# Kernel tuning notes

Measured on AMD Instinct MI355X. Metric: run time of the kernel, lower is better.

The kernel has to match this reference:

```python
import jax, jax.numpy as jnp
import numpy as np

REG1 = 0.5
REG2 = 0.5
ALPHA = 0.5

def setup_inputs() -> dict:
    key = jax.random.key(0)
    k1, k2, k3, k4, k5 = jax.random.split(key, 5)
    N, D, K = 32768, 256, 2048
    return {
        "encoder_out": jax.random.normal(k1, (N, D), dtype=jnp.float32),
        "prototypes": jax.random.normal(k2, (K, D), dtype=jnp.float32),
        "recon_loss": jax.random.uniform(k3, (), dtype=jnp.float32),
        "kl_loss": jax.random.uniform(k4, (), dtype=jnp.float32),
        "mmd_loss": jax.random.uniform(k5, (), dtype=jnp.float32),
    }


def _cdist_min_loss(z, prototypes):
    # torch.cdist(z, protos) -> [N, K]; f_dist = cdist(protos, z) = its transpose.
    # prototypes accessed via .data in torch -> detached.
    p = jax.lax.stop_gradient(prototypes)
    z2 = jnp.sum(z * z, axis=1, keepdims=True)          # [N, 1]
    p2 = jnp.sum(p * p, axis=1)                          # [K]
    sq = z2 + p2[None, :] - 2.0 * (z @ p.T)              # [N, K]
    dist = jnp.sqrt(jnp.maximum(sq, 0.0))
    p_min = jnp.min(dist, axis=1).mean()   # p_dist.min(1).values.mean()
    f_min = jnp.min(dist, axis=0).mean()   # f_dist [K,N].min(1) == dist.min(0)
    return REG1 * p_min + REG2 * f_min


def reference(encoder_out, prototypes, recon_loss, kl_loss, mmd_loss):
    cvae_loss = recon_loss + ALPHA * kl_loss + mmd_loss
    prot_decoding_loss = _cdist_min_loss(encoder_out, prototypes)
    # no projection head (use_projector=False)
    x = encoder_out / jnp.maximum(
        jnp.linalg.norm(encoder_out, axis=1, keepdims=True), 1e-12)
    x_mapped = x @ prototypes.T  # [N, K]
    return (encoder_out, x, x_mapped, cvae_loss, prot_decoding_loss)
```

## Files before the change

### kernel.cpp

```cpp
#include <hip/hip_runtime.h>
#include <hip/hip_bf16.h>

typedef __bf16 bf16x8 __attribute__((ext_vector_type(8)));
typedef __bf16 bf16x4 __attribute__((ext_vector_type(4)));
typedef float  f32x4  __attribute__((ext_vector_type(4)));

#define N_ROWS 32768
#define D_DIM  256
#define K_PROT 2048

#define WS_Z2    0
#define WS_INVN  32768
#define WS_P2    65536
#define WS_RMIN  67584
#define WS_CMIN  100352
#define WS_ZB    102400
#define WS_PB    (102400 + 4194304)

#define OUT_X0   0UL
#define OUT_X1   8388608UL
#define OUT_XMAP 16777216UL
#define OUT_CVAE 83886080UL
#define OUT_PROT 83886081UL

__device__ __forceinline__ void gload16(const __bf16* gsrc, const __bf16* ldst) {
    auto g = (const __attribute__((address_space(1))) unsigned int*)(unsigned long long)gsrc;
    auto l = (__attribute__((address_space(3))) unsigned int*)(unsigned long long)ldst;
    __builtin_amdgcn_global_load_lds(g, l, 16, 0, 0);
}

__global__ __launch_bounds__(256) void k12_rows(
    const float* __restrict__ Z, const float* __restrict__ P,
    float* __restrict__ out0, float* __restrict__ out1,
    float* __restrict__ z2, float* __restrict__ invn, unsigned int* __restrict__ rmin,
    __bf16* __restrict__ Zb,
    float* __restrict__ p2, unsigned int* __restrict__ cmin, __bf16* __restrict__ Pb)
{
    int b    = blockIdx.x;
    int lane = threadIdx.x & 63;
    if (b < (N_ROWS/4)) {
        int row  = (b << 2) + (threadIdx.x >> 6);
        size_t base = (size_t)row * D_DIM;
        float4 v = ((const float4*)(Z + base))[lane];
        float ss = v.x*v.x + v.y*v.y + v.z*v.z + v.w*v.w;
        #pragma unroll
        for (int d = 32; d >= 1; d >>= 1) ss += __shfl_xor(ss, d);
        float inv = 1.0f / fmaxf(sqrtf(ss), 1e-12f);
        ((float4*)(out0 + base))[lane] = v;
        float4 xv; xv.x = v.x*inv; xv.y = v.y*inv; xv.z = v.z*inv; xv.w = v.w*inv;
        ((float4*)(out1 + base))[lane] = xv;
        bf16x4 bv; bv[0]=(__bf16)v.x; bv[1]=(__bf16)v.y; bv[2]=(__bf16)v.z; bv[3]=(__bf16)v.w;
        ((bf16x4*)(Zb + base))[lane] = bv;
        if (lane == 0) { z2[row] = ss; invn[row] = inv; rmin[row] = 0x7f800000u; }
    } else {
        int row  = ((b - (N_ROWS/4)) << 2) + (threadIdx.x >> 6);
        size_t base = (size_t)row * D_DIM;
        float4 v = ((const float4*)(P + base))[lane];
        float ss = v.x*v.x + v.y*v.y + v.z*v.z + v.w*v.w;
        #pragma unroll
        for (int d = 32; d >= 1; d >>= 1) ss += __shfl_xor(ss, d);
        bf16x4 bv; bv[0]=(__bf16)v.x; bv[1]=(__bf16)v.y; bv[2]=(__bf16)v.z; bv[3]=(__bf16)v.w;
        ((bf16x4*)(Pb + base))[lane] = bv;
        if (lane == 0) { p2[row] = ss; cmin[row] = 0x7f800000u; }
    }
}

#define BM 128
#define BN 128
#define BK 64

__global__ __launch_bounds__(256, 2) void k3_gemm(
    const __bf16* __restrict__ Zb, const __bf16* __restrict__ Pb,
    const float* __restrict__ z2, const float* __restrict__ p2,
    const float* __restrict__ invn,
    float* __restrict__ xmap,
    unsigned int* __restrict__ rmin, unsigned int* __restrict__ cmin)
{
    __shared__ __bf16 As[BM * BK];
    __shared__ __bf16 Bs[BN * BK];

    const int tid  = threadIdx.x;
    const int wg   = (blockIdx.x & 7) * 512 + (blockIdx.x >> 3);
    const int bn   = wg & 15;
    const int bm   = wg >> 4;
    const int lane = tid & 63;
    const int wave = tid >> 6;
    const int wm   = wave >> 1;
    const int wn   = wave & 1;
    const int l15  = lane & 15;
    const int quad = lane >> 4;

    const int m0 = bm * BM;
    const int n0 = bn * BN;

    f32x4 acc[4][4];
    #pragma unroll
    for (int i = 0; i < 4; i++)
        #pragma unroll
        for (int j = 0; j < 4; j++)
            #pragma unroll
            for (int r = 0; r < 4; r++) acc[i][j][r] = 0.0f;

    const int ch_row[4] = {
        ((0*4 + wave)*64 + lane) >> 3, ((1*4 + wave)*64 + lane) >> 3,
        ((2*4 + wave)*64 + lane) >> 3, ((3*4 + wave)*64 + lane) >> 3 };
    const int ch_c = lane & 7;

    for (int kt = 0; kt < D_DIM; kt += BK) {
        #pragma unroll
        for (int it = 0; it < 4; it++) {
            const __bf16* aS = Zb + (size_t)(m0 + ch_row[it]) * D_DIM + kt + ch_c * 8;
            const __bf16* bS = Pb + (size_t)(n0 + ch_row[it]) * D_DIM + kt + ch_c * 8;
            gload16(aS, As + (it*4 + wave) * 512);
            gload16(bS, Bs + (it*4 + wave) * 512);
        }
        __syncthreads();

        #pragma unroll
        for (int s = 0; s < 2; s++) {
            bf16x8 af[4], bfr[4];
            #pragma unroll
            for (int i = 0; i < 4; i++)
                af[i] = *(const bf16x8*)(As + (wm*64 + i*16 + l15) * BK + s*32 + quad*8);
            #pragma unroll
            for (int j = 0; j < 4; j++)
                bfr[j] = *(const bf16x8*)(Bs + (wn*64 + j*16 + l15) * BK + s*32 + quad*8);
            #pragma unroll
            for (int i = 0; i < 4; i++)
                #pragma unroll
                for (int j = 0; j < 4; j++)
                    acc[i][j] = __builtin_amdgcn_mfma_f32_16x16x32_bf16(af[i], bfr[j], acc[i][j], 0, 0, 0);
        }
        __syncthreads();
    }

    float invr[16], zzr[16];
    #pragma unroll
    for (int i = 0; i < 4; i++)
        #pragma unroll
        for (int r = 0; r < 4; r++) {
            int gm = m0 + wm*64 + i*16 + quad*4 + r;
            invr[i*4+r] = invn[gm];
            zzr[i*4+r]  = z2[gm];
        }
    float pp[4];
    #pragma unroll
    for (int j = 0; j < 4; j++) pp[j] = p2[n0 + wn*64 + j*16 + l15];

    float cminv[4] = {3.0e38f, 3.0e38f, 3.0e38f, 3.0e38f};

    #pragma unroll
    for (int i = 0; i < 4; i++) {
        #pragma unroll
        for (int r = 0; r < 4; r++) {
            int gm = m0 + wm*64 + i*16 + quad*4 + r;
            float zi = zzr[i*4+r], iv = invr[i*4+r];
            size_t orow = (size_t)gm * K_PROT + n0 + wn*64 + l15;
            float rv = 3.0e38f;
            #pragma unroll
            for (int j = 0; j < 4; j++) {
                float g = acc[i][j][r];
                xmap[orow + j*16] = g * iv;
                float d2 = fmaxf(zi + pp[j] - 2.0f*g, 0.0f);
                rv = fminf(rv, d2);
                cminv[j] = fminf(cminv[j], d2);
            }
            #pragma unroll
            for (int s = 1; s < 16; s <<= 1) rv = fminf(rv, __shfl_xor(rv, s));
            if (l15 == 0) atomicMin(&rmin[gm], __float_as_uint(rv));
        }
    }
    #pragma unroll
    for (int j = 0; j < 4; j++) {
        float cv = cminv[j];
        cv = fminf(cv, __shfl_xor(cv, 16));
        cv = fminf(cv, __shfl_xor(cv, 32));
        if (quad == 0) atomicMin(&cmin[n0 + wn*64 + j*16 + l15], __float_as_uint(cv));
    }
}

__global__ __launch_bounds__(1024) void k4_final(
    const float* __restrict__ rminf, const float* __restrict__ cminf,
    const float* __restrict__ recon, const float* __restrict__ kl,
    const float* __restrict__ mmd, float* __restrict__ out)
{
    __shared__ float sr[16], sc[16];
    int tid = threadIdx.x;
    float a = 0.0f, b = 0.0f;
    for (int i = tid; i < N_ROWS; i += 1024) a += sqrtf(fmaxf(rminf[i], 0.0f));
    for (int i = tid; i < K_PROT; i += 1024) b += sqrtf(fmaxf(cminf[i], 0.0f));
    #pragma unroll
    for (int d = 32; d >= 1; d >>= 1) { a += __shfl_xor(a, d); b += __shfl_xor(b, d); }
    int w = tid >> 6, lane = tid & 63;
    if (lane == 0) { sr[w] = a; sc[w] = b; }
    __syncthreads();
    if (tid == 0) {
        float SA = 0.0f, SB = 0.0f;
        #pragma unroll
        for (int i = 0; i < 16; i++) { SA += sr[i]; SB += sc[i]; }
        out[OUT_CVAE] = recon[0] + 0.5f*kl[0] + mmd[0];
        out[OUT_PROT] = 0.5f*(SA / (float)N_ROWS) + 0.5f*(SB / (float)K_PROT);
    }
}

extern "C" void kernel_launch(void* const* d_in, const int* in_sizes, int n_in,
                              void* d_out, int out_size, void* d_ws, size_t ws_size,
                              hipStream_t stream)
{
    const float* Z     = (const float*)d_in[0];
    const float* P     = (const float*)d_in[1];
    const float* recon = (const float*)d_in[2];
    const float* kl    = (const float*)d_in[3];
    const float* mmd   = (const float*)d_in[4];
    float* out = (float*)d_out;
    float* ws  = (float*)d_ws;

    float* z2   = ws + WS_Z2;
    float* invn = ws + WS_INVN;
    float* p2   = ws + WS_P2;
    unsigned int* rmin = (unsigned int*)(ws + WS_RMIN);
    unsigned int* cmin = (unsigned int*)(ws + WS_CMIN);
    __bf16* Zb = (__bf16*)(ws + WS_ZB);
    __bf16* Pb = (__bf16*)(ws + WS_PB);

    hipLaunchKernelGGL(k12_rows, dim3(N_ROWS/4 + K_PROT/4), dim3(256), 0, stream,
                       Z, P, out + OUT_X0, out + OUT_X1, z2, invn, rmin, Zb, p2, cmin, Pb);
    hipLaunchKernelGGL(k3_gemm, dim3((N_ROWS/BM)*(K_PROT/BN)), dim3(256), 0, stream,
                       Zb, Pb, z2, p2, invn, out + OUT_XMAP, rmin, cmin);
    hipLaunchKernelGGL(k4_final, dim3(1), dim3(1024), 0, stream,
                       (const float*)rmin, (const float*)cmin, recon, kl, mmd, out);
}
```

Baseline: 437.3 us.

## Replace global atomicMin with per-tile partial minima and parallel reduction kernel

The GEMM epilogue no longer issues global atomicMin per row and column. Each block combines its wave partials in shared memory and writes per-tile row and column minima to workspace buffers. A new 80-block reduce kernel finishes the minima, takes sqrt, sums, and atomically adds into two accumulators, replacing the single-block final kernel. Launch bounds are raised to 3 blocks per CU, and one extra kernel launch is added along with about 4MB of partial-buffer traffic.

After: 432.7 us. No clear change (-1.1%).

```diff
diff --git a/kernel.cpp b/kernel.cpp
--- a/kernel.cpp
+++ b/kernel.cpp
@@ -12,10 +12,11 @@
 #define WS_Z2    0
 #define WS_INVN  32768
 #define WS_P2    65536
-#define WS_RMIN  67584
-#define WS_CMIN  100352
-#define WS_ZB    102400
-#define WS_PB    (102400 + 4194304)
+#define WS_ACC   67584
+#define WS_RP    67600
+#define WS_CP    (67600 + 524288)
+#define WS_ZB    (67600 + 1048576)
+#define WS_PB    (67600 + 1048576 + 4194304)
 
 #define OUT_X0   0UL
 #define OUT_X1   8388608UL
@@ -32,12 +33,14 @@
 __global__ __launch_bounds__(256) void k12_rows(
     const float* __restrict__ Z, const float* __restrict__ P,
     float* __restrict__ out0, float* __restrict__ out1,
-    float* __restrict__ z2, float* __restrict__ invn, unsigned int* __restrict__ rmin,
+    float* __restrict__ z2, float* __restrict__ invn,
     __bf16* __restrict__ Zb,
-    float* __restrict__ p2, unsigned int* __restrict__ cmin, __bf16* __restrict__ Pb)
+    float* __restrict__ p2, __bf16* __restrict__ Pb,
+    float* __restrict__ accw)
 {
     int b    = blockIdx.x;
     int lane = threadIdx.x & 63;
+    if (b == 0 && threadIdx.x < 2) accw[threadIdx.x] = 0.0f;
     if (b < (N_ROWS/4)) {
         int row  = (b << 2) + (threadIdx.x >> 6);
         size_t base = (size_t)row * D_DIM;
@@ -51,7 +54,7 @@
         ((float4*)(out1 + base))[lane] = xv;
         bf16x4 bv; bv[0]=(__bf16)v.x; bv[1]=(__bf16)v.y; bv[2]=(__bf16)v.z; bv[3]=(__bf16)v.w;
         ((bf16x4*)(Zb + base))[lane] = bv;
-        if (lane == 0) { z2[row] = ss; invn[row] = inv; rmin[row] = 0x7f800000u; }
+        if (lane == 0) { z2[row] = ss; invn[row] = inv; }
     } else {
         int row  = ((b - (N_ROWS/4)) << 2) + (threadIdx.x >> 6);
         size_t base = (size_t)row * D_DIM;
@@ -61,7 +64,7 @@
         for (int d = 32; d >= 1; d >>= 1) ss += __shfl_xor(ss, d);
         bf16x4 bv; bv[0]=(__bf16)v.x; bv[1]=(__bf16)v.y; bv[2]=(__bf16)v.z; bv[3]=(__bf16)v.w;
         ((bf16x4*)(Pb + base))[lane] = bv;
-        if (lane == 0) { p2[row] = ss; cmin[row] = 0x7f800000u; }
+        if (lane == 0) { p2[row] = ss; }
     }
 }
 
@@ -69,12 +72,12 @@
 #define BN 128
 #define BK 64
 
-__global__ __launch_bounds__(256, 2) void k3_gemm(
+__global__ __launch_bounds__(256, 3) void k3_gemm(
     const __bf16* __restrict__ Zb, const __bf16* __restrict__ Pb,
     const float* __restrict__ z2, const float* __restrict__ p2,
     const float* __restrict__ invn,
     float* __restrict__ xmap,
-    unsigned int* __restrict__ rmin, unsigned int* __restrict__ cmin)
+    float* __restrict__ rp, float* __restrict__ cp)
 {
     __shared__ __bf16 As[BM * BK];
     __shared__ __bf16 Bs[BN * BK];
@@ -148,6 +151,7 @@
     for (int j = 0; j < 4; j++) pp[j] = p2[n0 + wn*64 + j*16 + l15];
 
     float cminv[4] = {3.0e38f, 3.0e38f, 3.0e38f, 3.0e38f};
+    float rvv[16];
 
     #pragma unroll
     for (int i = 0; i < 4; i++) {
@@ -167,40 +171,103 @@
             }
             #pragma unroll
             for (int s = 1; s < 16; s <<= 1) rv = fminf(rv, __shfl_xor(rv, s));
-            if (l15 == 0) atomicMin(&rmin[gm], __float_as_uint(rv));
-        }
-    }
+            rvv[i*4+r] = rv;
+        }
+    }
+    float cvv[4];
     #pragma unroll
     for (int j = 0; j < 4; j++) {
         float cv = cminv[j];
         cv = fminf(cv, __shfl_xor(cv, 16));
         cv = fminf(cv, __shfl_xor(cv, 32));
-        if (quad == 0) atomicMin(&cmin[n0 + wn*64 + j*16 + l15], __float_as_uint(cv));
-    }
-}
-
-__global__ __launch_bounds__(1024) void k4_final(
-    const float* __restrict__ rminf, const float* __restrict__ cminf,
+        cvv[j] = cv;
+    }
+
+    float* srow = (float*)As;
+    float* scol = srow + 128;
+    if (wn == 0 && l15 == 0) {
+        #pragma unroll
+        for (int i = 0; i < 4; i++)
+            #pragma unroll
+            for (int r = 0; r < 4; r++)
+                srow[wm*64 + i*16 + quad*4 + r] = rvv[i*4+r];
+    }
+    if (wm == 0 && quad == 0) {
+        #pragma unroll
+        for (int j = 0; j < 4; j++) scol[wn*64 + j*16 + l15] = cvv[j];
+    }
+    __syncthreads();
+    if (wn == 1 && l15 == 0) {
+        #pragma unroll
+        for (int i = 0; i < 4; i++)
+            #pragma unroll
+            for (int r = 0; r < 4; r++) {
+                int idx = wm*64 + i*16 + quad*4 + r;
+                srow[idx] = fminf(srow[idx], rvv[i*4+r]);
+            }
+    }
+    if (wm == 1 && quad == 0) {
+        #pragma unroll
+        for (int j = 0; j < 4; j++) {
+            int c = wn*64 + j*16 + l15;
+            scol[c] = fminf(scol[c], cvv[j]);
+        }
+    }
+    __syncthreads();
+    if (tid < 128)       rp[(size_t)bn * N_ROWS + m0 + tid] = srow[tid];
+    else if (tid < 256)  cp[(size_t)bm * K_PROT + n0 + (tid - 128)] = scol[tid - 128];
+}
+
+__global__ __launch_bounds__(256) void k4_reduce(
+    const float* __restrict__ rp, const float* __restrict__ cp,
+    float* __restrict__ accw)
+{
+    __shared__ float sbuf[160];
+    int b = blockIdx.x, t = threadIdx.x;
+    int lane = t & 63, w = t >> 6;
+    if (b < 64) {
+        float a = 0.0f;
+        #pragma unroll
+        for (int rr = 0; rr < 2; rr++) {
+            int row = b*512 + rr*256 + t;
+            float m = 3.0e38f;
+            #pragma unroll
+            for (int k = 0; k < 16; k++) m = fminf(m, rp[(size_t)k * N_ROWS + row]);
+            a += sqrtf(m);
+        }
+        #pragma unroll
+        for (int d = 32; d >= 1; d >>= 1) a += __shfl_xor(a, d);
+        if (lane == 0) sbuf[w] = a;
+        __syncthreads();
+        if (t == 0) atomicAdd(accw + 0, sbuf[0] + sbuf[1] + sbuf[2] + sbuf[3]);
+    } else {
+        int col  = (b - 64) * 128 + (t & 127);
+        int half = t >> 7;
+        float m = 3.0e38f;
+        for (int k = half*128; k < half*128 + 128; k++)
+            m = fminf(m, cp[(size_t)k * K_PROT + col]);
+        if (half == 0) sbuf[t] = m;
+        __syncthreads();
+        if (half == 1) sbuf[t - 128] = fminf(sbuf[t - 128], m);
+        __syncthreads();
+        if (t < 128) {
+            float s = sqrtf(sbuf[t]);
+            #pragma unroll
+            for (int d = 32; d >= 1; d >>= 1) s += __shfl_xor(s, d);
+            if (lane == 0) sbuf[128 + (t >> 6)] = s;
+        }
+        __syncthreads();
+        if (t == 0) atomicAdd(accw + 1, sbuf[128] + sbuf[129]);
+    }
+}
+
+__global__ void k5_final(
+    const float* __restrict__ accw,
     const float* __restrict__ recon, const float* __restrict__ kl,
     const float* __restrict__ mmd, float* __restrict__ out)
 {
-    __shared__ float sr[16], sc[16];
-    int tid = threadIdx.x;
-    float a = 0.0f, b = 0.0f;
-    for (int i = tid; i < N_ROWS; i += 1024) a += sqrtf(fmaxf(rminf[i], 0.0f));
-    for (int i = tid; i < K_PROT; i += 1024) b += sqrtf(fmaxf(cminf[i], 0.0f));
-    #pragma unroll
-    for (int d = 32; d >= 1; d >>= 1) { a += __shfl_xor(a, d); b += __shfl_xor(b, d); }
-    int w = tid >> 6, lane = tid & 63;
-    if (lane == 0) { sr[w] = a; sc[w] = b; }
-    __syncthreads();
-    if (tid == 0) {
-        float SA = 0.0f, SB = 0.0f;
-        #pragma unroll
-        for (int i = 0; i < 16; i++) { SA += sr[i]; SB += sc[i]; }
-        out[OUT_CVAE] = recon[0] + 0.5f*kl[0] + mmd[0];
-        out[OUT_PROT] = 0.5f*(SA / (float)N_ROWS) + 0.5f*(SB / (float)K_PROT);
-    }
+    out[OUT_CVAE] = recon[0] + 0.5f*kl[0] + mmd[0];
+    out[OUT_PROT] = 0.5f*(accw[0] / (float)N_ROWS) + 0.5f*(accw[1] / (float)K_PROT);
 }
 
 extern "C" void kernel_launch(void* const* d_in, const int* in_sizes, int n_in,
@@ -218,15 +285,16 @@
     float* z2   = ws + WS_Z2;
     float* invn = ws + WS_INVN;
     float* p2   = ws + WS_P2;
-    unsigned int* rmin = (unsigned int*)(ws + WS_RMIN);
-    unsigned int* cmin = (unsigned int*)(ws + WS_CMIN);
+    float* accw = ws + WS_ACC;
+    float* rp   = ws + WS_RP;
+    float* cp   = ws + WS_CP;
     __bf16* Zb = (__bf16*)(ws + WS_ZB);
     __bf16* Pb = (__bf16*)(ws + WS_PB);
 
     hipLaunchKernelGGL(k12_rows, dim3(N_ROWS/4 + K_PROT/4), dim3(256), 0, stream,
-                       Z, P, out + OUT_X0, out + OUT_X1, z2, invn, rmin, Zb, p2, cmin, Pb);
+                       Z, P, out + OUT_X0, out + OUT_X1, z2, invn, Zb, p2, Pb, accw);
     hipLaunchKernelGGL(k3_gemm, dim3((N_ROWS/BM)*(K_PROT/BN)), dim3(256), 0, stream,
-                       Zb, Pb, z2, p2, invn, out + OUT_XMAP, rmin, cmin);
-    hipLaunchKernelGGL(k4_final, dim3(1), dim3(1024), 0, stream,
-                       (const float*)rmin, (const float*)cmin, recon, kl, mmd, out);
-}
+                       Zb, Pb, z2, p2, invn, out + OUT_XMAP, rp, cp);
+    hipLaunchKernelGGL(k4_reduce, dim3(80), dim3(256), 0, stream, rp, cp, accw);
+    hipLaunchKernelGGL(k5_final, dim3(1), dim3(1), 0, stream, accw, recon, kl, mmd, out);
+}
```
